# Optimization experiments

Measured on AMD Instinct MI355X. Metric: run time of the kernel, lower is better.

The kernel has to match this reference:

```python
import jax, jax.numpy as jnp
import numpy as np

NLON = 720  # output longitude points for irfft
B, C = 4, 8
LMAX, MMAX, NLAT = 360, 361, 361


def setup_inputs() -> dict:
    key = jax.random.key(0)
    kx, kd = jax.random.split(key)
    # x: real view of complex coeffs, shape [B, C, 2(vec comp), lmax, mmax, 2(re/im)]
    x = jax.random.normal(kx, (B, C, 2, LMAX, MMAX, 2), dtype=jnp.float32)
    # dpct: precomputed dLegendre buffer, shape [2, mmax, lmax, nlat]
    dpct = jax.random.normal(kd, (2, MMAX, LMAX, NLAT), dtype=jnp.float32) * 0.1
    return {"x": x, "dpct": dpct}


def reference(x, dpct):
    # split vector components and real/imag parts
    x0r = x[..., 0, :, :, 0]  # [..., lmax, mmax]
    x0i = x[..., 0, :, :, 1]
    x1r = x[..., 1, :, :, 0]
    x1i = x[..., 1, :, :, 1]
    d0 = dpct[0].astype(x.dtype)  # [mmax, lmax, nlat]
    d1 = dpct[1].astype(x.dtype)

    def ein(a, d):
        return jnp.einsum('...lm,mlk->...km', a, d)

    srl = ein(x0r, d0) - ein(x1i, d1)   # [..., nlat, mmax]
    sim = ein(x0i, d0) + ein(x1r, d1)
    trl = -ein(x0i, d1) - ein(x1r, d0)
    tim = ein(x0r, d1) - ein(x1i, d0)

    s = jax.lax.complex(srl, sim)
    t = jax.lax.complex(trl, tim)
    xs = jnp.stack((s, t), axis=-3)     # [..., 2, nlat, mmax] complex
    # inverse real FFT over longitude, 'forward' norm (no scaling on inverse)
    out = jnp.fft.irfft(xs, n=NLON, axis=-1, norm='forward')  # [..., 2, nlat, nlon]
    return out
```

## Files before the change

### kernel.cpp

```cpp
#include <hip/hip_runtime.h>
#include <hip/hip_bf16.h>
#include <math.h>

#define LMAX 360
#define MMAX 361
#define NLAT 361
#define NLON 720
#define BC   32
#define MT   (BC*2*NLAT)
#define QT   722
#define KP   736
#define NP   768
#define BM   128
#define BN   128
#define BK   32

typedef __attribute__((ext_vector_type(8))) short short8;
typedef __attribute__((ext_vector_type(4))) short short4v;
typedef __attribute__((ext_vector_type(4))) float f32x4;

static __device__ __forceinline__ short f2bf(float v) {
    __hip_bfloat16 h = __float2bfloat16(v);
    return *reinterpret_cast<short*>(&h);
}

__global__ __launch_bounds__(256) void sht_prep_x(
    const float* __restrict__ x, __hip_bfloat16* __restrict__ xT)
{
    const int m0 = blockIdx.x * 32;
    const int l0 = blockIdx.y * 64;
    const int bc = blockIdx.z >> 1, f = blockIdx.z & 1;
    __shared__ float2 tile[64][33];
    const float2* __restrict__ x2 = (const float2*)x;
    const int t = threadIdx.x;
    const int rm = t & 31, rl = t >> 5;

    #pragma unroll
    for (int r = 0; r < 8; ++r) {
        int l  = l0 + rl + r * 8;
        int mm = m0 + rm;
        float2 v = make_float2(0.f, 0.f);
        if (l < LMAX && mm < MMAX)
            v = x2[((size_t)(bc * 2 + f) * LMAX + l) * MMAX + mm];
        tile[rl + r * 8][rm] = v;
    }
    __syncthreads();

    const int tm = t >> 3, lg = t & 7;
    const int m = m0 + tm;
    if (m >= MMAX) return;
    const int lw = l0 + lg * 8;
    if (lw >= LMAX) return;

    short8 re, im;
    #pragma unroll
    for (int e = 0; e < 8; ++e) {
        float2 v = tile[lg * 8 + e][tm];
        re[e] = f2bf(v.x);
        im[e] = f2bf(v.y);
    }
    size_t mb = (size_t)m * (128 * LMAX);
    *(short8*)((short*)xT + mb + (size_t)((f * 2 + 0) * 32 + bc) * LMAX + lw) = re;
    *(short8*)((short*)xT + mb + (size_t)((f * 2 + 1) * 32 + bc) * LMAX + lw) = im;
}

__global__ __launch_bounds__(256, 2) void sht_gemm1(
    const float* __restrict__ dpct, const __hip_bfloat16* __restrict__ xT,
    __hip_bfloat16* __restrict__ interQ)
{
    const int m  = blockIdx.x;
    const int K0 = blockIdx.y * 192;

    __shared__ __align__(16) char AlsB[192 * 128];
    __shared__ __align__(16) char BlsB[128 * 128];

    const int t    = threadIdx.x;
    const int lane = t & 63;
    const int wave = t >> 6;
    const int wm = (wave >> 1) * 96;
    const int wn = (wave & 1) * 64;
    const int fr = lane & 15;
    const int lq = lane >> 4;

    int kqv[3], lbv[3];
    #pragma unroll
    for (int it = 0; it < 3; ++it) {
        int task = it * 256 + t;
        kqv[it] = task % 48;
        lbv[it] = task / 48;
    }
    const int cB    = t >> 1;
    const int plane = cB >> 5, bcq = cB & 31;
    const int g0B   = (t & 1) * 4;

    const int            srcT[8] = {0, 1, 2, 3, 3, 2, 1, 0};
    const unsigned short sgnT[8] = {0, 0, 0x8000, 0x8000, 0x8000, 0, 0x8000, 0};

    f32x4 acc[6][4];
    const f32x4 zero = {0.f, 0.f, 0.f, 0.f};
    #pragma unroll
    for (int i = 0; i < 6; ++i)
        #pragma unroll
        for (int j = 0; j < 4; ++j) acc[i][j] = zero;

    float4 apf[3][4];
    short8 bpf[4];

    auto loadA = [&](int ks) {
        int p = ks / 6, l0 = (ks % 6) * 64;
        #pragma unroll
        for (int it = 0; it < 3; ++it) {
            int kg = K0 + kqv[it] * 4;
            size_t rb = (((size_t)p * MMAX + m) * LMAX) * (size_t)NLAT + kg;
            #pragma unroll
            for (int j = 0; j < 4; ++j) {
                int lg2 = l0 + lbv[it] * 4 + j;
                float4 v = make_float4(0.f, 0.f, 0.f, 0.f);
                if (lg2 < LMAX) {
                    const float* src = dpct + rb + (size_t)lg2 * NLAT;
                    if (kg + 3 <= 360) {
                        v = *(const float4*)src;
                    } else if (kg <= 360) {
                        v.x = src[0];
                        if (kg + 1 <= 360) v.y = src[1];
                        if (kg + 2 <= 360) v.z = src[2];
                    }
                }
                apf[it][j] = v;
            }
        }
    };

    auto loadB = [&](int ks) {
        int p = ks / 6, l0 = (ks % 6) * 64;
        int src = srcT[p * 4 + plane];
        short sg = (short)sgnT[p * 4 + plane];
        const short* bbase = (const short*)xT + (size_t)m * (128 * LMAX) +
                             (size_t)(src * 32 + bcq) * LMAX;
        #pragma unroll
        for (int i = 0; i < 4; ++i) {
            int g   = g0B + i;
            int lg2 = l0 + g * 8;
            short8 v;
            if (lg2 < LMAX) {
                v = *(const short8*)(bbase + lg2);
                #pragma unroll
                for (int e = 0; e < 8; ++e) v[e] ^= sg;
            } else {
                #pragma unroll
                for (int e = 0; e < 8; ++e) v[e] = 0;
            }
            bpf[i] = v;
        }
    };

    loadA(0);
    loadB(0);

    for (int ks = 0; ks < 12; ++ks) {
        __syncthreads();

        #pragma unroll
        for (int it = 0; it < 3; ++it) {
            const int lb = lbv[it];
            const int gA = lb >> 1;
            const int ob = (lb & 1) << 3;
#define WRITE_A_ROW(JJ, E0, E1, E2, E3)                                        \
            {                                                                  \
                int kl = kqv[it] * 4 + JJ;                                     \
                short4v w;                                                     \
                w[0] = f2bf(E0); w[1] = f2bf(E1);                              \
                w[2] = f2bf(E2); w[3] = f2bf(E3);                              \
                *(short4v*)(AlsB + kl * 128 + ((gA ^ (kl & 7)) << 4) + ob) = w;\
            }
            WRITE_A_ROW(0, apf[it][0].x, apf[it][1].x, apf[it][2].x, apf[it][3].x)
            WRITE_A_ROW(1, apf[it][0].y, apf[it][1].y, apf[it][2].y, apf[it][3].y)
            WRITE_A_ROW(2, apf[it][0].z, apf[it][1].z, apf[it][2].z, apf[it][3].z)
            WRITE_A_ROW(3, apf[it][0].w, apf[it][1].w, apf[it][2].w, apf[it][3].w)
#undef WRITE_A_ROW
        }
        #pragma unroll
        for (int i = 0; i < 4; ++i) {
            int g = g0B + i;
            *(short8*)(BlsB + cB * 128 + ((g ^ (cB & 7)) << 4)) = bpf[i];
        }
        __syncthreads();

        if (ks < 11) { loadA(ks + 1); loadB(ks + 1); }

        #pragma unroll
        for (int kk = 0; kk < 2; ++kk) {
            short8 af[6], bg[4];
            const int g = kk * 4 + lq;
            #pragma unroll
            for (int mi = 0; mi < 6; ++mi) {
                int k = wm + mi * 16 + fr;
                af[mi] = *(const short8*)(AlsB + k * 128 + ((g ^ (k & 7)) << 4));
            }
            #pragma unroll
            for (int ni = 0; ni < 4; ++ni) {
                int c = wn + ni * 16 + fr;
                bg[ni] = *(const short8*)(BlsB + c * 128 + ((g ^ (c & 7)) << 4));
            }
            #pragma unroll
            for (int mi = 0; mi < 6; ++mi)
                #pragma unroll
                for (int ni = 0; ni < 4; ++ni)
                    acc[mi][ni] = __builtin_amdgcn_mfma_f32_16x16x32_bf16(
                        af[mi], bg[ni], acc[mi][ni], 0, 0, 0);
        }
    }

    #pragma unroll
    for (int mi = 0; mi < 6; ++mi) {
        int kr = K0 + wm + mi * 16 + lq * 4;
        #pragma unroll
        for (int ni = 0; ni < 4; ++ni) {
            int c = wn + ni * 16 + fr;
            int pl = c >> 5, bc = c & 31;
            int ri = pl & 1, tt = pl >> 1;
            size_t qb = (size_t)(2 * m + ri) * MT + (size_t)(bc * 2 + tt) * NLAT;
            #pragma unroll
            for (int r = 0; r < 4; ++r) {
                int k = kr + r;
                if (k < NLAT)
                    interQ[qb + k] = __float2bfloat16(acc[mi][ni][r]);
            }
        }
    }
}

__global__ __launch_bounds__(256) void sht_transpose(
    const __hip_bfloat16* __restrict__ inQ, __hip_bfloat16* __restrict__ outT)
{
    __shared__ __hip_bfloat16 tile[64][65];
    const int R0 = blockIdx.x * 64;
    const int q0 = blockIdx.y * 64;
    const int tx = threadIdx.x & 63;
    const int ty = threadIdx.x >> 6;
    const __hip_bfloat16 zv = __float2bfloat16(0.f);

    for (int qq = ty; qq < 64; qq += 4) {
        int q = q0 + qq;
        tile[qq][tx] = (q < QT) ? inQ[(size_t)q * MT + R0 + tx] : zv;
    }
    __syncthreads();
    if (q0 + tx < KP) {
        for (int rr = ty; rr < 64; rr += 4) {
            outT[(size_t)(R0 + rr) * KP + q0 + tx] = tile[tx][rr];
        }
    }
}

__global__ __launch_bounds__(256) void sht_make_w(__hip_bfloat16* __restrict__ W)
{
    const int idx = blockIdx.x * 256 + threadIdx.x;
    const int j = idx / KP;
    const int q = idx % KP;
    float v = 0.f;
    if (j < NLON && q < QT) {
        int m = q >> 1;
        float coef = (m == 0 || m == 360) ? 1.f : 2.f;
        int ph = (m * j) % 720;
        float ang = (float)ph * (float)(2.0 * M_PI / 720.0);
        float s, c;
        __sincosf(ang, &s, &c);
        v = (q & 1) ? (-coef * s) : (coef * c);
    }
    W[idx] = __float2bfloat16(v);
}

__global__ __launch_bounds__(256) void sht_gemm(
    const __hip_bfloat16* __restrict__ A,
    const __hip_bfloat16* __restrict__ W,
    float* __restrict__ out)
{
    __shared__ __align__(16) __hip_bfloat16 As[BM * BK];
    __shared__ __align__(16) __hip_bfloat16 Bs[BN * BK];
    const int t  = threadIdx.x;
    const int R0 = blockIdx.x * BM;
    const int J0 = blockIdx.y * BN;

    const int rowA = t >> 2;
    const int kc   = (t & 3) * 8;
    const int gr0  = min(R0 + rowA,      MT - 1);
    const int gr1  = min(R0 + rowA + 64, MT - 1);
    const __hip_bfloat16* pa0 = A + (size_t)gr0 * KP + kc;
    const __hip_bfloat16* pa1 = A + (size_t)gr1 * KP + kc;
    const __hip_bfloat16* pb0 = W + (size_t)(J0 + rowA) * KP + kc;
    const __hip_bfloat16* pb1 = W + (size_t)(J0 + rowA + 64) * KP + kc;

    const int lane = t & 63;
    const int wave = t >> 6;
    const int wm = (wave >> 1) * 64;
    const int wn = (wave & 1) * 64;
    const int fr = lane & 15;
    const int kg = (lane >> 4) * 8;

    f32x4 acc[4][4];
    const f32x4 zero = {0.f, 0.f, 0.f, 0.f};
    #pragma unroll
    for (int i = 0; i < 4; ++i)
        #pragma unroll
        for (int j = 0; j < 4; ++j) acc[i][j] = zero;

    short8 va0 = *(const short8*)pa0;
    short8 va1 = *(const short8*)pa1;
    short8 vb0 = *(const short8*)pb0;
    short8 vb1 = *(const short8*)pb1;

    for (int kt = 0; kt < KP / BK; ++kt) {
        __syncthreads();
        *(short8*)&As[t * 8]        = va0;
        *(short8*)&As[t * 8 + 2048] = va1;
        *(short8*)&Bs[t * 8]        = vb0;
        *(short8*)&Bs[t * 8 + 2048] = vb1;
        __syncthreads();

        if (kt + 1 < KP / BK) {
            const int ko = (kt + 1) * BK;
            va0 = *(const short8*)(pa0 + ko);
            va1 = *(const short8*)(pa1 + ko);
            vb0 = *(const short8*)(pb0 + ko);
            vb1 = *(const short8*)(pb1 + ko);
        }

        short8 af[4], bg[4];
        #pragma unroll
        for (int i = 0; i < 4; ++i)
            af[i] = *(const short8*)&As[(wm + i * 16 + fr) * BK + kg];
        #pragma unroll
        for (int i = 0; i < 4; ++i)
            bg[i] = *(const short8*)&Bs[(wn + i * 16 + fr) * BK + kg];

        #pragma unroll
        for (int mi = 0; mi < 4; ++mi)
            #pragma unroll
            for (int ni = 0; ni < 4; ++ni)
                acc[mi][ni] = __builtin_amdgcn_mfma_f32_16x16x32_bf16(
                    af[mi], bg[ni], acc[mi][ni], 0, 0, 0);
    }

    const int orow = (lane >> 4) * 4;
    #pragma unroll
    for (int mi = 0; mi < 4; ++mi) {
        #pragma unroll
        for (int ni = 0; ni < 4; ++ni) {
            #pragma unroll
            for (int r = 0; r < 4; ++r) {
                int row = R0 + wm + mi * 16 + orow + r;
                int col = J0 + wn + ni * 16 + fr;
                if (row < MT && col < NLON)
                    out[(size_t)row * NLON + col] = acc[mi][ni][r];
            }
        }
    }
}

extern "C" void kernel_launch(void* const* d_in, const int* in_sizes, int n_in,
                              void* d_out, int out_size, void* d_ws, size_t ws_size,
                              hipStream_t stream)
{
    const float* x    = (const float*)d_in[0];
    const float* dpct = (const float*)d_in[1];
    float* out        = (float*)d_out;

    char* ws = (char*)d_ws;
    __hip_bfloat16* xT     = (__hip_bfloat16*)ws;
    __hip_bfloat16* interT = (__hip_bfloat16*)ws;
    __hip_bfloat16* interQ = (__hip_bfloat16*)(ws + 34009088);
    __hip_bfloat16* Wt     = (__hip_bfloat16*)(ws + 34009088);

    dim3 gp(12, 6, 64);
    sht_prep_x<<<gp, 256, 0, stream>>>(x, xT);

    dim3 g1(MMAX, 2);
    sht_gemm1<<<g1, 256, 0, stream>>>(dpct, xT, interQ);

    dim3 gt(MT / 64, 12);
    sht_transpose<<<gt, 256, 0, stream>>>(interQ, interT);

    sht_make_w<<<(NP * KP) / 256, 256, 0, stream>>>(Wt);

    dim3 gg((MT + BM - 1) / BM, NP / BN);
    sht_gemm<<<gg, 256, 0, stream>>>(interT, Wt, out);
}
```

Measured before the change: 283.4 us.

## Halve gemm1 K-tile, double grid, and load dpct with k-contiguous lanes

The first Legendre GEMM now uses a 96-row latitude tile instead of 192, doubling the grid in y and raising the launch-bounds occupancy target to three blocks per CU. It also changes the dpct loading pattern. Each thread now reads eight scalar floats strided by NLAT, with consecutive threads on consecutive latitude indices for coalescing, replacing float4 vector loads, and writes one 16-byte swizzled LDS row per task. The aim is more parallelism and occupancy in a memory-bound GEMM, at the cost of more scalar load instructions and the xT B tile being reloaded by twice as many blocks.

```diff
diff --git a/kernel.cpp b/kernel.cpp
--- a/kernel.cpp
+++ b/kernel.cpp
@@ -16,7 +16,6 @@
 #define BK   32
 
 typedef __attribute__((ext_vector_type(8))) short short8;
-typedef __attribute__((ext_vector_type(4))) short short4v;
 typedef __attribute__((ext_vector_type(4))) float f32x4;
 
 static __device__ __forceinline__ short f2bf(float v) {
@@ -64,30 +63,30 @@
     *(short8*)((short*)xT + mb + (size_t)((f * 2 + 1) * 32 + bc) * LMAX + lw) = im;
 }
 
-__global__ __launch_bounds__(256, 2) void sht_gemm1(
+__global__ __launch_bounds__(256, 3) void sht_gemm1(
     const float* __restrict__ dpct, const __hip_bfloat16* __restrict__ xT,
     __hip_bfloat16* __restrict__ interQ)
 {
     const int m  = blockIdx.x;
-    const int K0 = blockIdx.y * 192;
-
-    __shared__ __align__(16) char AlsB[192 * 128];
+    const int K0 = blockIdx.y * 96;
+
+    __shared__ __align__(16) char AlsB[96 * 128];
     __shared__ __align__(16) char BlsB[128 * 128];
 
     const int t    = threadIdx.x;
     const int lane = t & 63;
     const int wave = t >> 6;
-    const int wm = (wave >> 1) * 96;
+    const int wm = (wave >> 1) * 48;
     const int wn = (wave & 1) * 64;
     const int fr = lane & 15;
     const int lq = lane >> 4;
 
-    int kqv[3], lbv[3];
+    int kdv[3], lov[3];
     #pragma unroll
     for (int it = 0; it < 3; ++it) {
         int task = it * 256 + t;
-        kqv[it] = task % 48;
-        lbv[it] = task / 48;
+        kdv[it] = task % 96;
+        lov[it] = task / 96;
     }
     const int cB    = t >> 1;
     const int plane = cB >> 5, bcq = cB & 31;
@@ -96,37 +95,29 @@
     const int            srcT[8] = {0, 1, 2, 3, 3, 2, 1, 0};
     const unsigned short sgnT[8] = {0, 0, 0x8000, 0x8000, 0x8000, 0, 0x8000, 0};
 
-    f32x4 acc[6][4];
+    f32x4 acc[3][4];
     const f32x4 zero = {0.f, 0.f, 0.f, 0.f};
     #pragma unroll
-    for (int i = 0; i < 6; ++i)
+    for (int i = 0; i < 3; ++i)
         #pragma unroll
         for (int j = 0; j < 4; ++j) acc[i][j] = zero;
 
-    float4 apf[3][4];
+    float  apf[3][8];
     short8 bpf[4];
 
     auto loadA = [&](int ks) {
         int p = ks / 6, l0 = (ks % 6) * 64;
         #pragma unroll
         for (int it = 0; it < 3; ++it) {
-            int kg = K0 + kqv[it] * 4;
-            size_t rb = (((size_t)p * MMAX + m) * LMAX) * (size_t)NLAT + kg;
-            #pragma unroll
-            for (int j = 0; j < 4; ++j) {
-                int lg2 = l0 + lbv[it] * 4 + j;
-                float4 v = make_float4(0.f, 0.f, 0.f, 0.f);
-                if (lg2 < LMAX) {
-                    const float* src = dpct + rb + (size_t)lg2 * NLAT;
-                    if (kg + 3 <= 360) {
-                        v = *(const float4*)src;
-                    } else if (kg <= 360) {
-                        v.x = src[0];
-                        if (kg + 1 <= 360) v.y = src[1];
-                        if (kg + 2 <= 360) v.z = src[2];
-                    }
-                }
-                apf[it][j] = v;
+            int kg = K0 + kdv[it];
+            bool kval = (kg <= 360);
+            int lb = l0 + lov[it] * 8;
+            bool lval = (lb < LMAX);
+            const float* src = dpct +
+                (((size_t)p * MMAX + m) * LMAX + lb) * (size_t)NLAT + kg;
+            #pragma unroll
+            for (int e = 0; e < 8; ++e) {
+                apf[it][e] = (kval && lval) ? src[(size_t)e * NLAT] : 0.f;
             }
         }
     };
@@ -162,22 +153,11 @@
 
         #pragma unroll
         for (int it = 0; it < 3; ++it) {
-            const int lb = lbv[it];
-            const int gA = lb >> 1;
-            const int ob = (lb & 1) << 3;
-#define WRITE_A_ROW(JJ, E0, E1, E2, E3)                                        \
-            {                                                                  \
-                int kl = kqv[it] * 4 + JJ;                                     \
-                short4v w;                                                     \
-                w[0] = f2bf(E0); w[1] = f2bf(E1);                              \
-                w[2] = f2bf(E2); w[3] = f2bf(E3);                              \
-                *(short4v*)(AlsB + kl * 128 + ((gA ^ (kl & 7)) << 4) + ob) = w;\
-            }
-            WRITE_A_ROW(0, apf[it][0].x, apf[it][1].x, apf[it][2].x, apf[it][3].x)
-            WRITE_A_ROW(1, apf[it][0].y, apf[it][1].y, apf[it][2].y, apf[it][3].y)
-            WRITE_A_ROW(2, apf[it][0].z, apf[it][1].z, apf[it][2].z, apf[it][3].z)
-            WRITE_A_ROW(3, apf[it][0].w, apf[it][1].w, apf[it][2].w, apf[it][3].w)
-#undef WRITE_A_ROW
+            short8 w;
+            #pragma unroll
+            for (int e = 0; e < 8; ++e) w[e] = f2bf(apf[it][e]);
+            int kd = kdv[it], lo = lov[it];
+            *(short8*)(AlsB + kd * 128 + ((lo ^ (kd & 7)) << 4)) = w;
         }
         #pragma unroll
         for (int i = 0; i < 4; ++i) {
@@ -190,10 +170,10 @@
 
         #pragma unroll
         for (int kk = 0; kk < 2; ++kk) {
-            short8 af[6], bg[4];
+            short8 af[3], bg[4];
             const int g = kk * 4 + lq;
             #pragma unroll
-            for (int mi = 0; mi < 6; ++mi) {
+            for (int mi = 0; mi < 3; ++mi) {
                 int k = wm + mi * 16 + fr;
                 af[mi] = *(const short8*)(AlsB + k * 128 + ((g ^ (k & 7)) << 4));
             }
@@ -203,7 +183,7 @@
                 bg[ni] = *(const short8*)(BlsB + c * 128 + ((g ^ (c & 7)) << 4));
             }
             #pragma unroll
-            for (int mi = 0; mi < 6; ++mi)
+            for (int mi = 0; mi < 3; ++mi)
                 #pragma unroll
                 for (int ni = 0; ni < 4; ++ni)
                     acc[mi][ni] = __builtin_amdgcn_mfma_f32_16x16x32_bf16(
@@ -212,7 +192,7 @@
     }
 
     #pragma unroll
-    for (int mi = 0; mi < 6; ++mi) {
+    for (int mi = 0; mi < 3; ++mi) {
         int kr = K0 + wm + mi * 16 + lq * 4;
         #pragma unroll
         for (int ni = 0; ni < 4; ++ni) {
@@ -374,7 +354,7 @@
     dim3 gp(12, 6, 64);
     sht_prep_x<<<gp, 256, 0, stream>>>(x, xT);
 
-    dim3 g1(MMAX, 2);
+    dim3 g1(MMAX, 4);
     sht_gemm1<<<g1, 256, 0, stream>>>(dpct, xT, interQ);
 
     dim3 gt(MT / 64, 12);
```

After: 299.2 us. 1.06x slower.

## Give each wave a private A slice and double-buffer B in gemm1

Applied to the files above, without the earlier changes.

Reworks the first GEMM so each wave owns a 48-row slice of the dpct tile, stored in a private padded LDS region with a new swizzle. Each wave loads and writes only its own A slice, so the A staging needs no block-wide barrier. The B tile becomes double-buffered, leaving one __syncthreads per K step instead of two, and the next loads overlap the MFMA work. Wave tiling changes from 96x64 to 48x128, so each wave reads all B columns from LDS. This raises LDS traffic for B and adds manual waitcnt and sched_barrier ordering.

```diff
diff --git a/kernel.cpp b/kernel.cpp
--- a/kernel.cpp
+++ b/kernel.cpp
@@ -71,23 +71,24 @@
     const int m  = blockIdx.x;
     const int K0 = blockIdx.y * 192;
 
-    __shared__ __align__(16) char AlsB[192 * 128];
-    __shared__ __align__(16) char BlsB[128 * 128];
+    __shared__ __align__(16) char Als[4 * 48 * 144];
+    __shared__ __align__(16) char Bls[2][128 * 128];
 
     const int t    = threadIdx.x;
     const int lane = t & 63;
     const int wave = t >> 6;
-    const int wm = (wave >> 1) * 96;
-    const int wn = (wave & 1) * 64;
+    const int wk   = K0 + wave * 48;
+    char* Aw = Als + wave * (48 * 144);
+
     const int fr = lane & 15;
     const int lq = lane >> 4;
 
     int kqv[3], lbv[3];
     #pragma unroll
     for (int it = 0; it < 3; ++it) {
-        int task = it * 256 + t;
-        kqv[it] = task % 48;
-        lbv[it] = task / 48;
+        int task = it * 64 + lane;
+        kqv[it] = task % 12;
+        lbv[it] = task / 12;
     }
     const int cB    = t >> 1;
     const int plane = cB >> 5, bcq = cB & 31;
@@ -96,28 +97,27 @@
     const int            srcT[8] = {0, 1, 2, 3, 3, 2, 1, 0};
     const unsigned short sgnT[8] = {0, 0, 0x8000, 0x8000, 0x8000, 0, 0x8000, 0};
 
-    f32x4 acc[6][4];
+    f32x4 acc[3][8];
     const f32x4 zero = {0.f, 0.f, 0.f, 0.f};
     #pragma unroll
-    for (int i = 0; i < 6; ++i)
-        #pragma unroll
-        for (int j = 0; j < 4; ++j) acc[i][j] = zero;
+    for (int i = 0; i < 3; ++i)
+        #pragma unroll
+        for (int j = 0; j < 8; ++j) acc[i][j] = zero;
 
     float4 apf[3][4];
     short8 bpf[4];
 
-    auto loadA = [&](int ks) {
-        int p = ks / 6, l0 = (ks % 6) * 64;
+    auto loadA = [&](int p, int l0) {
+        const size_t rowb = ((size_t)p * MMAX + m) * LMAX;
         #pragma unroll
         for (int it = 0; it < 3; ++it) {
-            int kg = K0 + kqv[it] * 4;
-            size_t rb = (((size_t)p * MMAX + m) * LMAX) * (size_t)NLAT + kg;
+            const int kg = wk + kqv[it] * 4;
             #pragma unroll
             for (int j = 0; j < 4; ++j) {
-                int lg2 = l0 + lbv[it] * 4 + j;
+                int l = l0 + lbv[it] * 4 + j;
                 float4 v = make_float4(0.f, 0.f, 0.f, 0.f);
-                if (lg2 < LMAX) {
-                    const float* src = dpct + rb + (size_t)lg2 * NLAT;
+                if (l < LMAX) {
+                    const float* src = dpct + (rowb + l) * (size_t)NLAT + kg;
                     if (kg + 3 <= 360) {
                         v = *(const float4*)src;
                     } else if (kg <= 360) {
@@ -131,8 +131,7 @@
         }
     };
 
-    auto loadB = [&](int ks) {
-        int p = ks / 6, l0 = (ks % 6) * 64;
+    auto loadB = [&](int p, int l0) {
         int src = srcT[p * 4 + plane];
         short sg = (short)sgnT[p * 4 + plane];
         const short* bbase = (const short*)xT + (size_t)m * (128 * LMAX) +
@@ -154,24 +153,17 @@
         }
     };
 
-    loadA(0);
-    loadB(0);
-
-    for (int ks = 0; ks < 12; ++ks) {
-        __syncthreads();
-
+    auto writeA = [&]() {
         #pragma unroll
         for (int it = 0; it < 3; ++it) {
             const int lb = lbv[it];
-            const int gA = lb >> 1;
-            const int ob = (lb & 1) << 3;
 #define WRITE_A_ROW(JJ, E0, E1, E2, E3)                                        \
             {                                                                  \
                 int kl = kqv[it] * 4 + JJ;                                     \
                 short4v w;                                                     \
                 w[0] = f2bf(E0); w[1] = f2bf(E1);                              \
                 w[2] = f2bf(E2); w[3] = f2bf(E3);                              \
-                *(short4v*)(AlsB + kl * 128 + ((gA ^ (kl & 7)) << 4) + ob) = w;\
+                *(short4v*)(Aw + kl * 144 + ((lb ^ (kl & 14)) << 3)) = w;      \
             }
             WRITE_A_ROW(0, apf[it][0].x, apf[it][1].x, apf[it][2].x, apf[it][3].x)
             WRITE_A_ROW(1, apf[it][0].y, apf[it][1].y, apf[it][2].y, apf[it][3].y)
@@ -179,44 +171,69 @@
             WRITE_A_ROW(3, apf[it][0].w, apf[it][1].w, apf[it][2].w, apf[it][3].w)
 #undef WRITE_A_ROW
         }
+    };
+
+    auto writeB = [&](char* Bb) {
         #pragma unroll
         for (int i = 0; i < 4; ++i) {
             int g = g0B + i;
-            *(short8*)(BlsB + cB * 128 + ((g ^ (cB & 7)) << 4)) = bpf[i];
-        }
-        __syncthreads();
-
-        if (ks < 11) { loadA(ks + 1); loadB(ks + 1); }
-
+            *(short8*)(Bb + cB * 128 + ((g ^ (cB & 7)) << 4)) = bpf[i];
+        }
+    };
+
+    loadB(0, 0);
+    loadA(0, 0);
+    writeB(&Bls[0][0]);
+    __syncthreads();
+
+    #pragma unroll 1
+    for (int s = 0; s < 12; ++s) {
+        const int pn  = (s + 1 >= 6) ? 1 : 0;
+        const int l0n = ((s + 1) % 6) * 64;
+
+        if (s < 11) loadB(pn, l0n);
+        writeA();
+        if (s < 11) loadA(pn, l0n);
+
+        asm volatile("s_waitcnt lgkmcnt(0)" ::: "memory");
+        __builtin_amdgcn_sched_barrier(0);
+
+        const char* Bb = &Bls[s & 1][0];
         #pragma unroll
         for (int kk = 0; kk < 2; ++kk) {
-            short8 af[6], bg[4];
-            const int g = kk * 4 + lq;
-            #pragma unroll
-            for (int mi = 0; mi < 6; ++mi) {
-                int k = wm + mi * 16 + fr;
-                af[mi] = *(const short8*)(AlsB + k * 128 + ((g ^ (k & 7)) << 4));
-            }
-            #pragma unroll
-            for (int ni = 0; ni < 4; ++ni) {
-                int c = wn + ni * 16 + fr;
-                bg[ni] = *(const short8*)(BlsB + c * 128 + ((g ^ (c & 7)) << 4));
-            }
-            #pragma unroll
-            for (int mi = 0; mi < 6; ++mi)
+            short8 af[3], bg[8];
+            const int g8  = (kk * 4 + lq) * 2;
+            const int g16 = kk * 4 + lq;
+            #pragma unroll
+            for (int mi = 0; mi < 3; ++mi) {
+                int kl = mi * 16 + fr;
+                af[mi] = *(const short8*)(Aw + kl * 144 + ((g8 ^ (kl & 14)) << 3));
+            }
+            #pragma unroll
+            for (int ni = 0; ni < 8; ++ni) {
+                int c = ni * 16 + fr;
+                bg[ni] = *(const short8*)(Bb + c * 128 + ((g16 ^ (c & 7)) << 4));
+            }
+            #pragma unroll
+            for (int mi = 0; mi < 3; ++mi)
                 #pragma unroll
-                for (int ni = 0; ni < 4; ++ni)
+                for (int ni = 0; ni < 8; ++ni)
                     acc[mi][ni] = __builtin_amdgcn_mfma_f32_16x16x32_bf16(
                         af[mi], bg[ni], acc[mi][ni], 0, 0, 0);
         }
-    }
-
-    #pragma unroll
-    for (int mi = 0; mi < 6; ++mi) {
-        int kr = K0 + wm + mi * 16 + lq * 4;
-        #pragma unroll
-        for (int ni = 0; ni < 4; ++ni) {
-            int c = wn + ni * 16 + fr;
+
+        if (s < 11) {
+            writeB(&Bls[(s + 1) & 1][0]);
+            __syncthreads();
+        }
+    }
+
+    #pragma unroll
+    for (int mi = 0; mi < 3; ++mi) {
+        int kr = wk + mi * 16 + lq * 4;
+        #pragma unroll
+        for (int ni = 0; ni < 8; ++ni) {
+            int c = ni * 16 + fr;
             int pl = c >> 5, bc = c & 31;
             int ri = pl & 1, tt = pl >> 1;
             size_t qb = (size_t)(2 * m + ri) * MT + (size_t)(bc * 2 + tt) * NLAT;
```

Measured after the change: 285.7 us. Within noise of the previous version (+0.8%).
